# Kernel tuning notes

Hardware: AMD Instinct MI355X
Metric: run time of the kernel (lower is better)

## Reference

```python
import jax, jax.numpy as jnp
import numpy as np

N_HEADS = 16
HEAD_DIM = 128  # d_model // n_heads


def rope(x):
    # x: [B, H, T, D]. Matches the torch module: interleaved even/odd split,
    # then concat([x1*cos - x2*sin, x1*sin + x2*cos], axis=-1).
    T, D = x.shape[2], x.shape[3]
    inv_freq = 1.0 / (10000.0 ** (jnp.arange(0, D, 2, dtype=x.dtype) / D))  # [D/2]
    freqs = jnp.arange(T, dtype=x.dtype)[:, None] * inv_freq[None, :]       # [T, D/2]
    sin, cos = jnp.sin(freqs), jnp.cos(freqs)                               # [T, D/2]
    x1, x2 = x[..., ::2], x[..., 1::2]                                      # [B,H,T,D/2]
    return jnp.concatenate([x1 * cos - x2 * sin, x1 * sin + x2 * cos], axis=-1)


def setup_inputs() -> dict:
    key = jax.random.key(0)
    ks = jax.random.split(key, 5)
    B, T, C = 2, 2048, 2048
    scale = 1.0 / np.sqrt(C)
    return {
        "x": jax.random.normal(ks[0], (B, T, C), dtype=jnp.float32),
        "W_qkv": jax.random.normal(ks[1], (3 * C, C), dtype=jnp.float32) * scale,
        "b_qkv": jnp.zeros((3 * C,), dtype=jnp.float32),
        "W_out": jax.random.normal(ks[2], (C, C), dtype=jnp.float32) * scale,
        "b_out": jnp.zeros((C,), dtype=jnp.float32),
    }


def reference(x, W_qkv, b_qkv, W_out, b_out):
    B, T, C = x.shape
    H, D = N_HEADS, HEAD_DIM
    qkv = x @ W_qkv.T + b_qkv                      # [B, T, 3C]
    qkv = qkv.reshape(B, T, 3, H, D)
    q, k, v = qkv[:, :, 0], qkv[:, :, 1], qkv[:, :, 2]  # [B, T, H, D]
    q = rope(jnp.transpose(q, (0, 2, 1, 3)))       # [B, H, T, D]
    k = rope(jnp.transpose(k, (0, 2, 1, 3)))
    v = jnp.transpose(v, (0, 2, 1, 3))
    scores = jnp.einsum("bhqd,bhkd->bhqk", q, k) / jnp.sqrt(jnp.asarray(D, x.dtype))
    causal = jnp.tril(jnp.ones((T, T), dtype=bool))
    scores = jnp.where(causal, scores, jnp.finfo(x.dtype).min)
    attn = jax.nn.softmax(scores, axis=-1)
    out = jnp.einsum("bhqk,bhkd->bhqd", attn, v)   # [B, H, T, D]
    out = jnp.transpose(out, (0, 2, 1, 3)).reshape(B, T, C)
    return out @ W_out.T + b_out
```

## Files before the change

kernel.cpp:

```cpp
#include <hip/hip_runtime.h>
#include <hip/hip_bf16.h>

typedef __attribute__((ext_vector_type(8))) short bf16x8;
typedef __attribute__((ext_vector_type(4))) float f32x4;

#define GLOAD_LDS16(gptr, lptr) \
  __builtin_amdgcn_global_load_lds((const __attribute__((address_space(1))) void*)(gptr), \
                                   (__attribute__((address_space(3))) void*)(lptr), 16, 0, 0)

__device__ __forceinline__ unsigned short f2b(float f) {
  union { float f; unsigned u; } x; x.f = f;
  unsigned r = x.u + 0x7fffu + ((x.u >> 16) & 1u);
  return (unsigned short)(r >> 16);
}
__device__ __forceinline__ float b2f(unsigned short u) {
  union { unsigned u; float f; } x; x.u = ((unsigned)u) << 16;
  return x.f;
}

__global__ void cast_kernel(const float* __restrict__ in, unsigned short* __restrict__ out, int n) {
  const int i = (blockIdx.x * 256 + threadIdx.x) * 4;
  if (i < n) {
    const float4 v = *(const float4*)(in + i);
    ushort4 r;
    r.x = f2b(v.x); r.y = f2b(v.y); r.z = f2b(v.z); r.w = f2b(v.w);
    *(ushort4*)(out + i) = r;
  }
}

template<int OUTF32>
__global__ __launch_bounds__(512, 2)
void gemm256(const unsigned short* __restrict__ A,
             const unsigned short* __restrict__ Bm,
             const float* __restrict__ bias,
             void* __restrict__ Cp,
             int M, int N, int K)
{
  __shared__ __align__(16) char Lds[131072];
  const int t  = threadIdx.x;
  const int l  = t & 63;
  const int w  = t >> 6;
  const int lr = l & 15;
  const int lkb = (l >> 4) << 4;
  const int wr = w >> 2;
  const int wc = w & 3;

  const int nwg = gridDim.x;
  const int wg  = (blockIdx.x & 7) * (nwg >> 3) + (blockIdx.x >> 3);
  const int NBN = N >> 8;
  const int bm = wg / NBN, bn = wg % NBN;

  const int sw3 = (lr & 7) << 4;
  const int ck0 = lkb ^ sw3;
  const int ck1 = (64 | lkb) ^ sw3;

  const int lb0 = t << 4;
  const int lb1 = lb0 + 8192;
  const int d0 = lb0 ^ (((lb0 >> 7) & 7) << 4);
  const int d1 = lb1 ^ (((lb1 >> 7) & 7) << 4);
  const long K2 = (long)K * 2;
  const char* Ab = (const char*)A  + (long)(bm * 256) * K2;
  const char* Bb = (const char*)Bm + (long)(bn * 256) * K2;
  const long s0 = (long)(d0 >> 7) * K2 + (d0 & 127);
  const long s1 = (long)(d1 >> 7) * K2 + (d1 & 127);
  const long hstep = (long)128 * K2;

  auto stageA = [&](int g, int h) {
    char* dst = Lds + (g & 1) * 65536 + h * 16384;
    const char* src = Ab + (long)h * hstep + (long)g * 128;
    GLOAD_LDS16(src + s0, dst + lb0);
    GLOAD_LDS16(src + s1, dst + lb1);
  };
  auto stageB = [&](int g, int h) {
    char* dst = Lds + (g & 1) * 65536 + 32768 + h * 16384;
    const char* src = Bb + (long)h * hstep + (long)g * 128;
    GLOAD_LDS16(src + s0, dst + lb0);
    GLOAD_LDS16(src + s1, dst + lb1);
  };

  f32x4 acc[8][4] = {};
  const int NT = K >> 6;

  stageA(0, 0); stageA(0, 1);
  stageB(0, 0); stageB(0, 1);
  stageB(1, 0); stageB(1, 1);
  asm volatile("s_waitcnt vmcnt(4)" ::: "memory");
  __builtin_amdgcn_s_barrier();

  const int brow = ((wc & 1) * 64 + lr) << 7;

  for (int tt = 0; tt < NT; ++tt) {
    const char* SB = Lds + (tt & 1) * 65536;
    const char* AH = SB + wr * 16384;
    const char* BH = SB + 32768 + (wc >> 1) * 16384;
    bf16x8 af[4][2], blo[2][2], bhi[2][2];

#pragma unroll
    for (int mi = 0; mi < 4; ++mi) {
      af[mi][0] = *(const bf16x8*)(AH + ((mi * 16 + lr) << 7) + ck0);
      af[mi][1] = *(const bf16x8*)(AH + ((mi * 16 + lr) << 7) + ck1);
    }
#pragma unroll
    for (int ni = 0; ni < 2; ++ni) {
      blo[ni][0] = *(const bf16x8*)(BH + brow + (ni << 11) + ck0);
      blo[ni][1] = *(const bf16x8*)(BH + brow + (ni << 11) + ck1);
    }
    if (tt + 1 < NT) stageA(tt + 1, 0);
    __builtin_amdgcn_s_barrier();
    asm volatile("s_waitcnt lgkmcnt(0)" ::: "memory");
    __builtin_amdgcn_sched_barrier(0);
    __builtin_amdgcn_s_setprio(1);
#pragma unroll
    for (int mi = 0; mi < 4; ++mi)
#pragma unroll
      for (int ni = 0; ni < 2; ++ni) {
        acc[mi][ni] = __builtin_amdgcn_mfma_f32_16x16x32_bf16(af[mi][0], blo[ni][0], acc[mi][ni], 0, 0, 0);
        acc[mi][ni] = __builtin_amdgcn_mfma_f32_16x16x32_bf16(af[mi][1], blo[ni][1], acc[mi][ni], 0, 0, 0);
      }
    __builtin_amdgcn_s_setprio(0);
    __builtin_amdgcn_s_barrier();

#pragma unroll
    for (int ni = 0; ni < 2; ++ni) {
      bhi[ni][0] = *(const bf16x8*)(BH + brow + ((ni + 2) << 11) + ck0);
      bhi[ni][1] = *(const bf16x8*)(BH + brow + ((ni + 2) << 11) + ck1);
    }
    if (tt + 1 < NT) stageA(tt + 1, 1);
    __builtin_amdgcn_s_barrier();
    asm volatile("s_waitcnt lgkmcnt(0)" ::: "memory");
    __builtin_amdgcn_sched_barrier(0);
    __builtin_amdgcn_s_setprio(1);
#pragma unroll
    for (int mi = 0; mi < 4; ++mi)
#pragma unroll
      for (int ni = 0; ni < 2; ++ni) {
        acc[mi][ni + 2] = __builtin_amdgcn_mfma_f32_16x16x32_bf16(af[mi][0], bhi[ni][0], acc[mi][ni + 2], 0, 0, 0);
        acc[mi][ni + 2] = __builtin_amdgcn_mfma_f32_16x16x32_bf16(af[mi][1], bhi[ni][1], acc[mi][ni + 2], 0, 0, 0);
      }
    __builtin_amdgcn_s_setprio(0);
    __builtin_amdgcn_s_barrier();

#pragma unroll
    for (int mi = 0; mi < 4; ++mi) {
      af[mi][0] = *(const bf16x8*)(AH + ((64 + mi * 16 + lr) << 7) + ck0);
      af[mi][1] = *(const bf16x8*)(AH + ((64 + mi * 16 + lr) << 7) + ck1);
    }
    if (tt + 2 < NT) stageB(tt + 2, 0);
    __builtin_amdgcn_s_barrier();
    asm volatile("s_waitcnt lgkmcnt(0)" ::: "memory");
    __builtin_amdgcn_sched_barrier(0);
    __builtin_amdgcn_s_setprio(1);
#pragma unroll
    for (int mi = 0; mi < 4; ++mi)
#pragma unroll
      for (int ni = 0; ni < 2; ++ni) {
        acc[mi + 4][ni] = __builtin_amdgcn_mfma_f32_16x16x32_bf16(af[mi][0], blo[ni][0], acc[mi + 4][ni], 0, 0, 0);
        acc[mi + 4][ni] = __builtin_amdgcn_mfma_f32_16x16x32_bf16(af[mi][1], blo[ni][1], acc[mi + 4][ni], 0, 0, 0);
      }
    __builtin_amdgcn_s_setprio(0);
    __builtin_amdgcn_s_barrier();

    if (tt + 2 < NT) stageB(tt + 2, 1);
    __builtin_amdgcn_s_setprio(1);
#pragma unroll
    for (int mi = 0; mi < 4; ++mi)
#pragma unroll
      for (int ni = 0; ni < 2; ++ni) {
        acc[mi + 4][ni + 2] = __builtin_amdgcn_mfma_f32_16x16x32_bf16(af[mi][0], bhi[ni][0], acc[mi + 4][ni + 2], 0, 0, 0);
        acc[mi + 4][ni + 2] = __builtin_amdgcn_mfma_f32_16x16x32_bf16(af[mi][1], bhi[ni][1], acc[mi + 4][ni + 2], 0, 0, 0);
      }
    __builtin_amdgcn_s_setprio(0);
    asm volatile("s_waitcnt vmcnt(4)" ::: "memory");
    __builtin_amdgcn_s_barrier();
  }

  const int roff = (l >> 4) << 2;
  const int row0 = bm * 256 + wr * 128 + roff;
  const int col0 = bn * 256 + wc * 64 + lr;
#pragma unroll
  for (int ni = 0; ni < 4; ++ni) {
    const int col = col0 + ni * 16;
    const float bv = bias ? bias[col] : 0.0f;
#pragma unroll
    for (int mi = 0; mi < 8; ++mi) {
#pragma unroll
      for (int r = 0; r < 4; ++r) {
        const int row = row0 + mi * 16 + r;
        const float v = acc[mi][ni][r] + bv;
        if (OUTF32) ((float*)Cp)[(long)row * N + col] = v;
        else ((unsigned short*)Cp)[(long)row * N + col] = f2b(v);
      }
    }
  }
}

__global__ void rope_kernel(const unsigned short* __restrict__ qkv,
                            unsigned short* __restrict__ Qr,
                            unsigned short* __restrict__ Kr)
{
  const int T = 2048;
  const int idx = blockIdx.x * 256 + threadIdx.x;
  const int d  = idx & 63;
  const int tt = (idx >> 6) & (T - 1);
  const int bh = idx >> 17;
  const int b = bh >> 4, h = bh & 15;
  const long base = ((long)(b * T + tt) * 3) * 2048 + h * 128;
  const float inv = exp2f(-(float)d * 0.2076205059304602f);
  const float fr = (float)tt * inv;
  float sn, cs;
  sincosf(fr, &sn, &cs);
  const float q1 = b2f(qkv[base + 2 * d]);
  const float q2 = b2f(qkv[base + 2 * d + 1]);
  const float k1 = b2f(qkv[base + 2048 + 2 * d]);
  const float k2 = b2f(qkv[base + 2048 + 2 * d + 1]);
  const long ob = ((long)bh * T + tt) * 128;
  Qr[ob + d]      = f2b(q1 * cs - q2 * sn);
  Qr[ob + 64 + d] = f2b(q1 * sn + q2 * cs);
  Kr[ob + d]      = f2b(k1 * cs - k2 * sn);
  Kr[ob + 64 + d] = f2b(k1 * sn + k2 * cs);
}

__global__ void vtrans_kernel(const unsigned short* __restrict__ qkv,
                              unsigned short* __restrict__ Vt)
{
  const int T = 2048;
  __shared__ unsigned short ld[128][65];
  const int bh = blockIdx.y, tt = blockIdx.x;
  const int b = bh >> 4, h = bh & 15;
  const int t = threadIdx.x;
#pragma unroll
  for (int i = 0; i < 32; ++i) {
    const int idx = i * 256 + t;
    const int d = idx & 127, tr = idx >> 7;
    ld[d][tr] = qkv[((long)(b * T + tt * 64 + tr) * 3 + 2) * 2048 + h * 128 + d];
  }
  __syncthreads();
#pragma unroll
  for (int i = 0; i < 32; ++i) {
    const int idx = i * 256 + t;
    const int tc = idx & 63, dr = idx >> 6;
    Vt[((long)bh * 128 + dr) * T + tt * 64 + tc] = ld[dr][tc];
  }
}

__global__ __launch_bounds__(256)
void attn_fwd(const unsigned short* __restrict__ Q,
              const unsigned short* __restrict__ Kg,
              const unsigned short* __restrict__ Vt,
              unsigned short* __restrict__ O, int T)
{
  __shared__ __align__(16) unsigned short Ks[2][64 * 128];
  __shared__ __align__(16) unsigned short Vs[2][128 * 64];
  __shared__ __align__(16) unsigned short Ps[4][16 * 64];
  const int t = threadIdx.x;
  const int w = t >> 6, l = t & 63;
  const int lr = l & 15;
  const int g16 = (l >> 4) << 4;
  const int sw = (lr & 7) << 4;
  const int bh = blockIdx.x;
  const int qt = (gridDim.y - 1) - blockIdx.y;
  const int q0 = qt * 64 + w * 16;
  const long hbase = (long)bh * T * 128;
  const long hbase2 = hbase * 2;
  const long T2 = (long)T * 2;
  const int roff = (l >> 4) << 2;

  bf16x8 qf[4];
  const unsigned short* Qrow = Q + hbase + (long)(q0 + lr) * 128;
#pragma unroll
  for (int ds = 0; ds < 4; ++ds) qf[ds] = *(const bf16x8*)&Qrow[ds * 32 + (g16 >> 1)];

  f32x4 o[8] = {};
  float m[4]    = {-INFINITY, -INFINITY, -INFINITY, -INFINITY};
  float lsum[4] = {0.f, 0.f, 0.f, 0.f};

  auto stage = [&](int kt, int buf) {
#pragma unroll
    for (int c = 0; c < 4; ++c) {
      const int o2 = t * 16 + c * 4096;
      const int krow = o2 >> 8, kcb = o2 & 255;
      GLOAD_LDS16((const char*)Kg + hbase2 + (long)kt * 16384 + krow * 256 + (kcb ^ ((krow & 7) << 4)),
                  (char*)Ks[buf] + o2);
      const int vrow = o2 >> 7, vcb = o2 & 127;
      GLOAD_LDS16((const char*)Vt + (long)(bh * 128 + vrow) * T2 + (long)kt * 128 + (vcb ^ ((vrow & 7) << 4)),
                  (char*)Vs[buf] + o2);
    }
  };

  const int ntile = qt + 1;
  stage(0, 0);
  __syncthreads();

  for (int kt = 0; kt < ntile; ++kt) {
    const int cur = kt & 1;
    if (kt + 1 < ntile) stage(kt + 1, cur ^ 1);

    const char* KsB = (const char*)Ks[cur];
    const char* VsB = (const char*)Vs[cur];

    f32x4 s[4] = {};
    __builtin_amdgcn_s_setprio(1);
#pragma unroll
    for (int tj = 0; tj < 4; ++tj)
#pragma unroll
      for (int ds = 0; ds < 4; ++ds) {
        bf16x8 kf = *(const bf16x8*)(KsB + (tj * 16 + lr) * 256 + ((ds * 64 + g16) ^ sw));
        s[tj] = __builtin_amdgcn_mfma_f32_16x16x32_bf16(qf[ds], kf, s[tj], 0, 0, 0);
      }
    __builtin_amdgcn_s_setprio(0);

    const float scale = 0.08838834764831845f;
#pragma unroll
    for (int tj = 0; tj < 4; ++tj) s[tj] *= scale;
    if (kt == qt) {
#pragma unroll
      for (int tj = 0; tj < 4; ++tj)
#pragma unroll
        for (int j = 0; j < 4; ++j)
          if (kt * 64 + tj * 16 + lr > q0 + roff + j) s[tj][j] = -INFINITY;
    }

    float corr[4];
#pragma unroll
    for (int j = 0; j < 4; ++j) {
      float v = fmaxf(fmaxf(s[0][j], s[1][j]), fmaxf(s[2][j], s[3][j]));
      v = fmaxf(v, __shfl_xor(v, 1, 64));
      v = fmaxf(v, __shfl_xor(v, 2, 64));
      v = fmaxf(v, __shfl_xor(v, 4, 64));
      v = fmaxf(v, __shfl_xor(v, 8, 64));
      const float mn = fmaxf(m[j], v);
      corr[j] = __expf(m[j] - mn);
      m[j] = mn;
    }
    float rs[4] = {0.f, 0.f, 0.f, 0.f};
#pragma unroll
    for (int tj = 0; tj < 4; ++tj)
#pragma unroll
      for (int j = 0; j < 4; ++j) {
        const float p = __expf(s[tj][j] - m[j]);
        rs[j] += p;
        const int prow = roff + j;
        *(unsigned short*)((char*)Ps[w] + prow * 128 + (((tj * 16 + lr) * 2) ^ ((prow & 7) << 4))) = f2b(p);
      }
#pragma unroll
    for (int j = 0; j < 4; ++j) {
      float v = rs[j];
      v += __shfl_xor(v, 1, 64);
      v += __shfl_xor(v, 2, 64);
      v += __shfl_xor(v, 4, 64);
      v += __shfl_xor(v, 8, 64);
      lsum[j] = lsum[j] * corr[j] + v;
    }
#pragma unroll
    for (int nj = 0; nj < 8; ++nj)
#pragma unroll
      for (int j = 0; j < 4; ++j) o[nj][j] *= corr[j];

    __builtin_amdgcn_s_setprio(1);
#pragma unroll
    for (int ks = 0; ks < 2; ++ks) {
      bf16x8 pf = *(const bf16x8*)((const char*)Ps[w] + lr * 128 + ((ks * 64 + g16) ^ sw));
#pragma unroll
      for (int nj = 0; nj < 8; ++nj) {
        bf16x8 vf = *(const bf16x8*)(VsB + (nj * 16 + lr) * 128 + ((ks * 64 + g16) ^ sw));
        o[nj] = __builtin_amdgcn_mfma_f32_16x16x32_bf16(pf, vf, o[nj], 0, 0, 0);
      }
    }
    __builtin_amdgcn_s_setprio(0);
    __syncthreads();
  }

  float inv[4];
#pragma unroll
  for (int j = 0; j < 4; ++j) inv[j] = 1.0f / lsum[j];
  const int b = bh >> 4, h = bh & 15;
#pragma unroll
  for (int nj = 0; nj < 8; ++nj)
#pragma unroll
    for (int j = 0; j < 4; ++j) {
      const int q = q0 + roff + j;
      const int d = nj * 16 + lr;
      O[(long)(b * T + q) * 2048 + h * 128 + d] = f2b(o[nj][j] * inv[j]);
    }
}

extern "C" void kernel_launch(void* const* d_in, const int* in_sizes, int n_in,
                              void* d_out, int out_size, void* d_ws, size_t ws_size,
                              hipStream_t stream)
{
  const int B = 2, T = 2048, C = 2048;
  const int M = B * T;
  const int N1 = 3 * C;
  const float* x    = (const float*)d_in[0];
  const float* Wqkv = (const float*)d_in[1];
  const float* bqkv = (const float*)d_in[2];
  const float* Wout = (const float*)d_in[3];
  const float* bout = (const float*)d_in[4];
  float* out = (float*)d_out;

  char* p = (char*)d_ws;
  unsigned short* xb    = (unsigned short*)p; p += (size_t)M * C * 2;
  unsigned short* wqkvb = (unsigned short*)p; p += (size_t)N1 * C * 2;
  unsigned short* woutb = (unsigned short*)p; p += (size_t)C * C * 2;
  unsigned short* qkv   = (unsigned short*)p; p += (size_t)M * N1 * 2;
  unsigned short* Qr    = (unsigned short*)p; p += (size_t)M * C * 2;
  unsigned short* Kr    = (unsigned short*)p; p += (size_t)M * C * 2;
  unsigned short* Vt    = (unsigned short*)p; p += (size_t)M * C * 2;
  unsigned short* Ob    = xb;

  cast_kernel<<<M * C / 1024, 256, 0, stream>>>(x, xb, M * C);
  cast_kernel<<<N1 * C / 1024, 256, 0, stream>>>(Wqkv, wqkvb, N1 * C);
  cast_kernel<<<C * C / 1024, 256, 0, stream>>>(Wout, woutb, C * C);

  gemm256<0><<<dim3((M / 256) * (N1 / 256)), 512, 0, stream>>>(xb, wqkvb, bqkv, qkv, M, N1, C);

  rope_kernel<<<(32 * T * 64) / 256, 256, 0, stream>>>(qkv, Qr, Kr);
  vtrans_kernel<<<dim3(T / 64, 32), 256, 0, stream>>>(qkv, Vt);

  attn_fwd<<<dim3(32, T / 64), 256, 0, stream>>>(Qr, Kr, Vt, Ob, T);

  gemm256<1><<<dim3((M / 256) * (C / 256)), 512, 0, stream>>>(Ob, woutb, bout, out, M, C, C);
}
```

Measured before the change: 323.5 us.

## Software-pipeline LDS fragment loads across iterations and cut barriers in GEMM loop

The GEMM main loop now loads the next K-tile's A and B fragments from shared memory (LDS) into registers during the current tile's MFMA phases. This replaces the earlier scheme, which loaded fragments at the start of each phase and then waited on lgkmcnt. Both A-half global→LDS stages are issued together at the top of the iteration, one of the per-phase barriers is dropped, and the vmcnt wait becomes a full vmcnt(0) in mid-iteration. The goal is to hide LDS read latency behind matrix math and reduce synchronisation stalls. The cost is more live registers, and the next-tile B fragment read may run before a barrier confirms other waves' global-to-LDS copies have landed.

```diff
diff --git a/kernel.cpp b/kernel.cpp
--- a/kernel.cpp
+++ b/kernel.cpp
@@ -80,34 +80,41 @@
 
   f32x4 acc[8][4] = {};
   const int NT = K >> 6;
+  const int brow = ((wc & 1) * 64 + lr) << 7;
+
+  bf16x8 af[4][2], blo[2][2], bhi[2][2];
 
   stageA(0, 0); stageA(0, 1);
   stageB(0, 0); stageB(0, 1);
   stageB(1, 0); stageB(1, 1);
   asm volatile("s_waitcnt vmcnt(4)" ::: "memory");
   __builtin_amdgcn_s_barrier();
-
-  const int brow = ((wc & 1) * 64 + lr) << 7;
+  {
+    const char* AH0 = Lds + wr * 16384;
+    const char* BH0 = Lds + 32768 + (wc >> 1) * 16384;
+#pragma unroll
+    for (int ni = 0; ni < 2; ++ni) {
+      blo[ni][0] = *(const bf16x8*)(BH0 + brow + (ni << 11) + ck0);
+      blo[ni][1] = *(const bf16x8*)(BH0 + brow + (ni << 11) + ck1);
+    }
+#pragma unroll
+    for (int mi = 0; mi < 4; ++mi) {
+      af[mi][0] = *(const bf16x8*)(AH0 + ((mi * 16 + lr) << 7) + ck0);
+      af[mi][1] = *(const bf16x8*)(AH0 + ((mi * 16 + lr) << 7) + ck1);
+    }
+#pragma unroll
+    for (int ni = 0; ni < 2; ++ni) {
+      bhi[ni][0] = *(const bf16x8*)(BH0 + brow + ((ni + 2) << 11) + ck0);
+      bhi[ni][1] = *(const bf16x8*)(BH0 + brow + ((ni + 2) << 11) + ck1);
+    }
+  }
 
   for (int tt = 0; tt < NT; ++tt) {
     const char* SB = Lds + (tt & 1) * 65536;
     const char* AH = SB + wr * 16384;
-    const char* BH = SB + 32768 + (wc >> 1) * 16384;
-    bf16x8 af[4][2], blo[2][2], bhi[2][2];
-
-#pragma unroll
-    for (int mi = 0; mi < 4; ++mi) {
-      af[mi][0] = *(const bf16x8*)(AH + ((mi * 16 + lr) << 7) + ck0);
-      af[mi][1] = *(const bf16x8*)(AH + ((mi * 16 + lr) << 7) + ck1);
-    }
-#pragma unroll
-    for (int ni = 0; ni < 2; ++ni) {
-      blo[ni][0] = *(const bf16x8*)(BH + brow + (ni << 11) + ck0);
-      blo[ni][1] = *(const bf16x8*)(BH + brow + (ni << 11) + ck1);
-    }
-    if (tt + 1 < NT) stageA(tt + 1, 0);
+
+    if (tt + 1 < NT) { stageA(tt + 1, 0); stageA(tt + 1, 1); }
     __builtin_amdgcn_s_barrier();
-    asm volatile("s_waitcnt lgkmcnt(0)" ::: "memory");
     __builtin_amdgcn_sched_barrier(0);
     __builtin_amdgcn_s_setprio(1);
 #pragma unroll
@@ -119,16 +126,8 @@
       }
     __builtin_amdgcn_s_setprio(0);
     __builtin_amdgcn_s_barrier();
-
-#pragma unroll
-    for (int ni = 0; ni < 2; ++ni) {
-      bhi[ni][0] = *(const bf16x8*)(BH + brow + ((ni + 2) << 11) + ck0);
-      bhi[ni][1] = *(const bf16x8*)(BH + brow + ((ni + 2) << 11) + ck1);
-    }
-    if (tt + 1 < NT) stageA(tt + 1, 1);
-    __builtin_amdgcn_s_barrier();
-    asm volatile("s_waitcnt lgkmcnt(0)" ::: "memory");
     __builtin_amdgcn_sched_barrier(0);
+
     __builtin_amdgcn_s_setprio(1);
 #pragma unroll
     for (int mi = 0; mi < 4; ++mi)
@@ -138,17 +137,16 @@
         acc[mi][ni + 2] = __builtin_amdgcn_mfma_f32_16x16x32_bf16(af[mi][1], bhi[ni][1], acc[mi][ni + 2], 0, 0, 0);
       }
     __builtin_amdgcn_s_setprio(0);
-    __builtin_amdgcn_s_barrier();
-
 #pragma unroll
     for (int mi = 0; mi < 4; ++mi) {
       af[mi][0] = *(const bf16x8*)(AH + ((64 + mi * 16 + lr) << 7) + ck0);
       af[mi][1] = *(const bf16x8*)(AH + ((64 + mi * 16 + lr) << 7) + ck1);
     }
+    __builtin_amdgcn_s_barrier();
+    __builtin_amdgcn_sched_barrier(0);
+
+    asm volatile("s_waitcnt vmcnt(0)" ::: "memory");
     if (tt + 2 < NT) stageB(tt + 2, 0);
-    __builtin_amdgcn_s_barrier();
-    asm volatile("s_waitcnt lgkmcnt(0)" ::: "memory");
-    __builtin_amdgcn_sched_barrier(0);
     __builtin_amdgcn_s_setprio(1);
 #pragma unroll
     for (int mi = 0; mi < 4; ++mi)
@@ -158,7 +156,16 @@
         acc[mi + 4][ni] = __builtin_amdgcn_mfma_f32_16x16x32_bf16(af[mi][1], blo[ni][1], acc[mi + 4][ni], 0, 0, 0);
       }
     __builtin_amdgcn_s_setprio(0);
+    if (tt + 1 < NT) {
+      const char* BHn = Lds + ((tt + 1) & 1) * 65536 + 32768 + (wc >> 1) * 16384;
+#pragma unroll
+      for (int ni = 0; ni < 2; ++ni) {
+        blo[ni][0] = *(const bf16x8*)(BHn + brow + (ni << 11) + ck0);
+        blo[ni][1] = *(const bf16x8*)(BHn + brow + (ni << 11) + ck1);
+      }
+    }
     __builtin_amdgcn_s_barrier();
+    __builtin_amdgcn_sched_barrier(0);
 
     if (tt + 2 < NT) stageB(tt + 2, 1);
     __builtin_amdgcn_s_setprio(1);
@@ -170,8 +177,23 @@
         acc[mi + 4][ni + 2] = __builtin_amdgcn_mfma_f32_16x16x32_bf16(af[mi][1], bhi[ni][1], acc[mi + 4][ni + 2], 0, 0, 0);
       }
     __builtin_amdgcn_s_setprio(0);
-    asm volatile("s_waitcnt vmcnt(4)" ::: "memory");
+    if (tt + 1 < NT) {
+      const char* SBn = Lds + ((tt + 1) & 1) * 65536;
+      const char* AHn = SBn + wr * 16384;
+      const char* BHn = SBn + 32768 + (wc >> 1) * 16384;
+#pragma unroll
+      for (int mi = 0; mi < 4; ++mi) {
+        af[mi][0] = *(const bf16x8*)(AHn + ((mi * 16 + lr) << 7) + ck0);
+        af[mi][1] = *(const bf16x8*)(AHn + ((mi * 16 + lr) << 7) + ck1);
+      }
+#pragma unroll
+      for (int ni = 0; ni < 2; ++ni) {
+        bhi[ni][0] = *(const bf16x8*)(BHn + brow + ((ni + 2) << 11) + ck0);
+        bhi[ni][1] = *(const bf16x8*)(BHn + brow + ((ni + 2) << 11) + ck1);
+      }
+    }
     __builtin_amdgcn_s_barrier();
+    __builtin_amdgcn_sched_barrier(0);
   }
 
   const int roff = (l >> 4) << 2;
```

Result: no change. 321.0 us (-0.8%).
